# Performance work log

Measured on AMD Instinct MI355X. Metric: run time of the kernel, lower is better.

Reference implementation:

```python
import jax, jax.numpy as jnp
import numpy as np

NUM_HEADS = 16
ROPE_BASE = 10000.0
MAX_POS = 4096


def _rope_tables(head_dim):
    inv_freq = 1.0 / (ROPE_BASE ** (np.arange(0, head_dim, 2, dtype=np.float32) / head_dim))
    freqs = np.arange(MAX_POS, dtype=np.float32)[:, None] * inv_freq[None, :]
    emb = np.concatenate([freqs, freqs], axis=-1)  # [MAX_POS, head_dim]
    return jnp.asarray(np.cos(emb)), jnp.asarray(np.sin(emb))


def _rotate_half(x):
    d = x.shape[-1] // 2
    return jnp.concatenate([-x[..., d:], x[..., :d]], axis=-1)


def _apply_rope(x, pos, cos_t, sin_t):
    # x: [B,H,S,D], pos: [B,S]
    cos = cos_t[pos][:, None]  # [B,1,S,D]
    sin = sin_t[pos][:, None]
    return x * cos + _rotate_half(x) * sin


def setup_inputs() -> dict:
    key = jax.random.key(0)
    ks = jax.random.split(key, 8)
    B, N, M, C = 2, 2048, 2048, 1024
    s = 1.0 / np.sqrt(C)
    return {
        "query": jax.random.normal(ks[0], (B, N, C), jnp.float32),
        "key": jax.random.normal(ks[1], (B, M, C), jnp.float32),
        "query_pos": jnp.broadcast_to(jnp.arange(N, dtype=jnp.int32), (B, N)),
        "key_pos": jnp.broadcast_to(jnp.arange(M, dtype=jnp.int32), (B, M)),
        "Wq": jax.random.normal(ks[2], (C, C), jnp.float32) * s,
        "bq": jnp.zeros((C,), jnp.float32),
        "Wk": jax.random.normal(ks[3], (C, C), jnp.float32) * s,
        "Wv": jax.random.normal(ks[4], (C, C), jnp.float32) * s,
        "bv": jnp.zeros((C,), jnp.float32),
        "Wo": jax.random.normal(ks[5], (C, C), jnp.float32) * s,
        "bo": jnp.zeros((C,), jnp.float32),
    }


def reference(query, key, query_pos, key_pos, Wq, bq, Wk, Wv, bv, Wo, bo):
    B, N, C = query.shape
    M = key.shape[1]
    H = NUM_HEADS
    D = C // H
    scale = D ** -0.5
    cos_t, sin_t = _rope_tables(D)

    value = key  # value defaults to key
    identity = query

    q = (query @ Wq.T + bq).reshape(B, N, H, D).transpose(0, 2, 1, 3)
    k = (key @ Wk.T).reshape(B, M, H, D).transpose(0, 2, 1, 3)
    v = (value @ Wv.T + bv).reshape(B, M, H, D).transpose(0, 2, 1, 3)

    q = _apply_rope(q, query_pos, cos_t, sin_t)
    k = _apply_rope(k, key_pos, cos_t, sin_t)

    attn = jnp.einsum('bhnd,bhmd->bhnm', q, k) * scale
    attn = jax.nn.softmax(attn, axis=-1)
    x = jnp.einsum('bhnm,bhmd->bhnd', attn, v)  # [B,H,N,D]
    x = x.transpose(0, 2, 1, 3).reshape(B, N, C)
    x = x @ Wo.T + bo
    return x + identity
```

## Files before the change

### kernel.cpp

```cpp
#include <hip/hip_runtime.h>
#include <hip/hip_bf16.h>
#include <stdint.h>

#define B_ 2
#define N_ 2048
#define M_ 2048
#define C_ 1024
#define H_ 16
#define D_ 64

typedef __attribute__((ext_vector_type(8))) short s16x8;
typedef __attribute__((ext_vector_type(4))) short s16x4;
typedef __attribute__((ext_vector_type(4))) float f32x4;
typedef __attribute__((ext_vector_type(16))) float f32x16;

__device__ __attribute__((always_inline)) inline short f2b(float f){
    __hip_bfloat16 h = __float2bfloat16(f); short s; __builtin_memcpy(&s, &h, 2); return s;
}
__device__ __attribute__((always_inline)) inline float b2f(short s){
    __hip_bfloat16 h; __builtin_memcpy(&h, &s, 2); return __bfloat162float(h);
}

#define MFMA16(a,b,c) __builtin_amdgcn_mfma_f32_16x16x32_bf16(a,b,c,0,0,0)
#define MFMA32(a,b,c) __builtin_amdgcn_mfma_f32_32x32x16_bf16(a,b,c,0,0,0)

__device__ __attribute__((always_inline)) inline void gl_lds16(const void* g, void* l){
    __builtin_amdgcn_global_load_lds((__attribute__((address_space(1))) void*)g,
                                     (__attribute__((address_space(3))) void*)l, 16, 0, 0);
}
__device__ __attribute__((always_inline)) inline unsigned fbits(float f){
    unsigned u; __builtin_memcpy(&u, &f, 4); return u;
}
__device__ __attribute__((always_inline)) inline unsigned cvtpk(float lo, float hi){
    unsigned r;
    asm("v_cvt_pk_bf16_f32 %0, %1, %2" : "=v"(r) : "v"(lo), "v"(hi));
    return r;
}
__device__ __attribute__((always_inline)) inline void lane32swap(unsigned &a, unsigned &b){
    asm("v_permlane32_swap_b32 %0, %1" : "+v"(a), "+v"(b));
}

__global__ void cvt_all(const float* __restrict__ q, const float* __restrict__ k,
                        const float* __restrict__ wq, const float* __restrict__ wk,
                        const float* __restrict__ wv, const float* __restrict__ wo,
                        short* __restrict__ dst){
    long i = ((long)blockIdx.x * 256 + threadIdx.x) * 8;
    const float* src; long off;
    if      (i <  4194304L){ src = q;  off = i; }
    else if (i <  8388608L){ src = k;  off = i - 4194304L; }
    else if (i <  9437184L){ src = wq; off = i - 8388608L; }
    else if (i < 10485760L){ src = wk; off = i - 9437184L; }
    else if (i < 11534336L){ src = wv; off = i - 10485760L; }
    else                   { src = wo; off = i - 11534336L; }
    float4 a = *(const float4*)(src + off);
    float4 b = *(const float4*)(src + off + 4);
    s16x8 o;
    o[0]=f2b(a.x); o[1]=f2b(a.y); o[2]=f2b(a.z); o[3]=f2b(a.w);
    o[4]=f2b(b.x); o[5]=f2b(b.y); o[6]=f2b(b.z); o[7]=f2b(b.w);
    *(s16x8*)(dst + i) = o;
}

__global__ __launch_bounds__(256, 3) void gemm_qkv(
    const short* __restrict__ qbf, const short* __restrict__ kbf,
    const short* __restrict__ W,
    const float* __restrict__ bq, const float* __restrict__ bv,
    short* __restrict__ qproj, short* __restrict__ kproj, short* __restrict__ vT)
{
    __shared__ short As[128 * 32];
    __shared__ short Bs[128 * 32];
    const int n0 = blockIdx.x * 128, m0 = blockIdx.y * 128;
    const int sel = n0 >> 10;
    const short* A = (sel == 0) ? qbf : kbf;
    const int tid = threadIdx.x, lane = tid & 63, wave = tid >> 6;
    const int quad = lane >> 4, l16 = lane & 15;
    const int wr = (wave >> 1) * 64, wc = (wave & 1) * 64;
    const int srow = lane >> 2, scol = (lane & 3) * 8;

    f32x4 acc[4][4] = {};

    const short* Ag = A + (size_t)(m0 + wave * 32 + srow) * C_ + scol;
    const short* Bg = W + (size_t)(n0 + wave * 32 + srow) * C_ + scol;
    short* lA0 = As + (wave * 32) * 32;
    short* lA1 = As + (wave * 32 + 16) * 32;
    short* lB0 = Bs + (wave * 32) * 32;
    short* lB1 = Bs + (wave * 32 + 16) * 32;

    for (int k0 = 0; k0 < C_; k0 += 32){
        __syncthreads();
        gl_lds16(Ag + k0, lA0);
        gl_lds16(Ag + k0 + 16 * (size_t)C_, lA1);
        gl_lds16(Bg + k0, lB0);
        gl_lds16(Bg + k0 + 16 * (size_t)C_, lB1);
        __syncthreads();
        s16x8 af[4], bfr[4];
        #pragma unroll
        for (int t = 0; t < 4; t++) af[t]  = *(const s16x8*)&As[(wr + t*16 + l16) * 32 + quad * 8];
        #pragma unroll
        for (int t = 0; t < 4; t++) bfr[t] = *(const s16x8*)&Bs[(wc + t*16 + l16) * 32 + quad * 8];
        #pragma unroll
        for (int i = 0; i < 4; i++)
            #pragma unroll
            for (int j = 0; j < 4; j++)
                acc[i][j] = MFMA16(af[i], bfr[j], acc[i][j]);
    }

    if (sel <= 1){
        short* dst = sel ? kproj : qproj;
        const float* bp = sel ? nullptr : bq;
        const int coff = sel << 10;
        #pragma unroll
        for (int j = 0; j < 4; j++){
            int c = n0 + wc + j * 16 + l16 - coff;
            float bb = bp ? bp[c] : 0.0f;
            #pragma unroll
            for (int i = 0; i < 4; i++){
                int row = m0 + wr + i * 16 + quad * 4;
                #pragma unroll
                for (int r = 0; r < 4; r++)
                    dst[(size_t)(row + r) * C_ + c] = f2b(acc[i][j][r] + bb);
            }
        }
    } else {
        #pragma unroll
        for (int j = 0; j < 4; j++){
            int col = n0 - 2048 + wc + j * 16 + l16;
            int h = col >> 6, d = col & 63;
            float bb = bv[col];
            #pragma unroll
            for (int i = 0; i < 4; i++){
                int row = m0 + wr + i * 16 + quad * 4;
                int b = row >> 11, m = row & 2047;
                unsigned u0 = (unsigned)(unsigned short)f2b(acc[i][j][0] + bb) |
                              ((unsigned)(unsigned short)f2b(acc[i][j][1] + bb) << 16);
                unsigned u1 = (unsigned)(unsigned short)f2b(acc[i][j][2] + bb) |
                              ((unsigned)(unsigned short)f2b(acc[i][j][3] + bb) << 16);
                uint2 u; u.x = u0; u.y = u1;
                *(uint2*)&vT[(((size_t)(b * H_ + h)) * D_ + d) * M_ + m] = u;
            }
        }
    }
}

__global__ __launch_bounds__(256, 4) void gemm_out(
    const short* __restrict__ A, const short* __restrict__ W,
    const float* __restrict__ bias, const float* __restrict__ resid,
    float* __restrict__ outf)
{
    __shared__ short As[128 * 32];
    __shared__ short Bs[64 * 32];
    const int n0 = blockIdx.x * 64, m0 = blockIdx.y * 128;
    const int tid = threadIdx.x, lane = tid & 63, wave = tid >> 6;
    const int quad = lane >> 4, l16 = lane & 15;
    const int srow = lane >> 2, scol = (lane & 3) * 8;

    f32x4 acc[2][4] = {};
    const short* Ag = A + (size_t)(m0 + wave * 32 + srow) * C_ + scol;
    const short* Bg = W + (size_t)(n0 + wave * 16 + srow) * C_ + scol;
    short* lA0 = As + (wave * 32) * 32;
    short* lA1 = As + (wave * 32 + 16) * 32;
    short* lB  = Bs + (wave * 16) * 32;

    for (int k0 = 0; k0 < C_; k0 += 32){
        __syncthreads();
        gl_lds16(Ag + k0, lA0);
        gl_lds16(Ag + k0 + 16 * (size_t)C_, lA1);
        gl_lds16(Bg + k0, lB);
        __syncthreads();
        s16x8 af[2], bfr[4];
        #pragma unroll
        for (int t = 0; t < 2; t++) af[t]  = *(const s16x8*)&As[(wave*32 + t*16 + l16) * 32 + quad * 8];
        #pragma unroll
        for (int t = 0; t < 4; t++) bfr[t] = *(const s16x8*)&Bs[(t*16 + l16) * 32 + quad * 8];
        #pragma unroll
        for (int i = 0; i < 2; i++)
            #pragma unroll
            for (int j = 0; j < 4; j++)
                acc[i][j] = MFMA16(af[i], bfr[j], acc[i][j]);
    }

    #pragma unroll
    for (int j = 0; j < 4; j++){
        int c = n0 + j * 16 + l16;
        float bb = bias[c];
        #pragma unroll
        for (int i = 0; i < 2; i++){
            int row = m0 + wave * 32 + i * 16 + quad * 4;
            #pragma unroll
            for (int r = 0; r < 4; r++){
                size_t idx = (size_t)(row + r) * C_ + c;
                outf[idx] = acc[i][j][r] + bb + resid[idx];
            }
        }
    }
}

__global__ void rope_k(short* __restrict__ k, const int* __restrict__ kpos){
    int t = blockIdx.x * blockDim.x + threadIdx.x;
    int i = t & 31;
    int h = (t >> 5) & (H_ - 1);
    int row = t >> 9;
    int pos = kpos[row];
    short* base = k + (size_t)row * C_ + h * D_;
    float x1 = b2f(base[i]), x2 = b2f(base[i + 32]);
    float invf = exp2f((float)i * (-13.287712379549449f / 32.0f));
    float f = (float)pos * invf;
    float c = __cosf(f), s = __sinf(f);
    base[i]      = f2b(x1 * c - x2 * s);
    base[i + 32] = f2b(x2 * c + x1 * s);
}

__global__ __launch_bounds__(256, 2) void flash_attn(
    const short* __restrict__ q, const short* __restrict__ k,
    const short* __restrict__ vt, short* __restrict__ o,
    const int* __restrict__ qpos)
{
    __shared__ short smem[17920];
    const int b = blockIdx.y >> 4, h = blockIdx.y & 15;
    const int n0 = blockIdx.x * 128;
    const int tid = threadIdx.x, lane = tid & 63, wave = tid >> 6;
    const int hi = lane >> 5, l32 = lane & 31;
    const int wq = wave & 1, kq = wave >> 1;

    s16x8 qf[2][4];
    const float fac = 0.18033688011112042f;
    #pragma unroll
    for (int qt = 0; qt < 2; qt++){
        int qrow = n0 + wq * 64 + qt * 32 + l32;
        const short* qg = &q[((size_t)(b * N_ + qrow)) * C_ + h * D_];
        float pos = (float)qpos[b * N_ + qrow];
        s16x8 raw[4];
        #pragma unroll
        for (int c = 0; c < 4; c++) raw[c] = *(const s16x8*)&qg[c * 16 + hi * 8];
        #pragma unroll
        for (int c = 0; c < 2; c++){
            s16x8 olo, ohi8;
            #pragma unroll
            for (int j = 0; j < 8; j++){
                int irot = c * 16 + hi * 8 + j;
                float invf = exp2f((float)irot * (-13.287712379549449f / 32.0f));
                float ang = pos * invf;
                float cs = __cosf(ang), sn = __sinf(ang);
                float x1 = b2f(raw[c][j]), x2 = b2f(raw[c + 2][j]);
                olo[j]  = f2b((x1 * cs - x2 * sn) * fac);
                ohi8[j] = f2b((x2 * cs + x1 * sn) * fac);
            }
            qf[qt][c] = olo; qf[qt][c + 2] = ohi8;
        }
    }

    const short* kg = k  + (size_t)(b * M_) * C_ + h * D_;
    const short* vg = vt + ((size_t)(b * H_ + h)) * D_ * M_;
    const int srow0 = tid >> 3, sseg = (tid & 7) * 8;

    union V8 { s16x8 v; uint2 u[2]; };
    V8 kreg[2], vreg[2];

    #pragma unroll
    for (int ii = 0; ii < 2; ii++){
        int row = srow0 + 32 * ii;
        kreg[ii].v = *(const s16x8*)&kg[(size_t)row * C_ + sseg];
        vreg[ii].v = *(const s16x8*)&vg[(size_t)row * M_ + sseg];
    }
    #pragma unroll
    for (int ii = 0; ii < 2; ii++){
        int row = srow0 + 32 * ii;
        short* kd = &smem[row * 68 + sseg];
        *(uint2*)kd = kreg[ii].u[0]; *(uint2*)(kd + 4) = kreg[ii].u[1];
        short* vd = &smem[8704 + row * 68 + sseg];
        *(uint2*)vd = vreg[ii].u[0]; *(uint2*)(vd + 4) = vreg[ii].u[1];
    }

    f32x16 zero16 = {};
    f32x16 oacc[2][2] = {zero16, zero16, zero16, zero16};
    float lacc[2] = {0.f, 0.f};

    for (int st = 0; st < 32; st++){
        const int p = st & 1;
        __syncthreads();
        if (st < 31){
            #pragma unroll
            for (int ii = 0; ii < 2; ii++){
                int row = srow0 + 32 * ii;
                kreg[ii].v = *(const s16x8*)&kg[((size_t)((st + 1) * 64 + row)) * C_ + sseg];
                vreg[ii].v = *(const s16x8*)&vg[(size_t)row * M_ + (st + 1) * 64 + sseg];
            }
        }
        const short* Kp = &smem[p * 4352];
        const short* Vp = &smem[8704 + p * 4352];

        s16x4 kf[4][2];
        #pragma unroll
        for (int c = 0; c < 4; c++){
            const short* a = &Kp[(kq * 32 + l32) * 68 + c * 16 + hi * 8];
            kf[c][0] = *(const s16x4*)a; kf[c][1] = *(const s16x4*)(a + 4);
        }
        s16x8 vf[2][2];
        #pragma unroll
        for (int dt = 0; dt < 2; dt++)
            #pragma unroll
            for (int c = 0; c < 2; c++){
                const short* a = &Vp[(dt * 32 + l32) * 68 + kq * 32 + c * 16 + hi * 8];
                vf[dt][c] = __builtin_shufflevector(*(const s16x4*)a, *(const s16x4*)(a + 4),
                                                    0,1,2,3,4,5,6,7);
            }

        s16x8 pf[2][2];
        #pragma unroll
        for (int qt = 0; qt < 2; qt++){
            f32x16 sv = {};
            #pragma unroll
            for (int c = 0; c < 4; c++){
                s16x8 ka = __builtin_shufflevector(kf[c][0], kf[c][1], 0,1,2,3,4,5,6,7);
                sv = MFMA32(ka, qf[qt][c], sv);
            }
            float pe[16];
            #pragma unroll
            for (int e = 0; e < 16; e++) pe[e] = __builtin_amdgcn_exp2f(sv[e]);
            float ls = 0.f;
            #pragma unroll
            for (int e = 0; e < 16; e += 4) ls += (pe[e] + pe[e+1]) + (pe[e+2] + pe[e+3]);
            lacc[qt] += ls;
            #pragma unroll
            for (int c = 0; c < 2; c++){
                unsigned a1 = cvtpk(pe[8*c + 0], pe[8*c + 1]);
                unsigned a2 = cvtpk(pe[8*c + 2], pe[8*c + 3]);
                unsigned b1 = cvtpk(pe[8*c + 4], pe[8*c + 5]);
                unsigned b2 = cvtpk(pe[8*c + 6], pe[8*c + 7]);
                lane32swap(a1, b1);
                lane32swap(a2, b2);
                union { unsigned u[4]; s16x8 v; } pk;
                pk.u[0] = a1; pk.u[1] = a2; pk.u[2] = b1; pk.u[3] = b2;
                pf[qt][c] = pk.v;
            }
        }

        #pragma unroll
        for (int qt = 0; qt < 2; qt++)
            #pragma unroll
            for (int dt = 0; dt < 2; dt++)
                #pragma unroll
                for (int c = 0; c < 2; c++)
                    oacc[qt][dt] = MFMA32(pf[qt][c], vf[dt][c], oacc[qt][dt]);

        if (st < 31){
            int pn = p ^ 1;
            #pragma unroll
            for (int ii = 0; ii < 2; ii++){
                int row = srow0 + 32 * ii;
                short* kd = &smem[pn * 4352 + row * 68 + sseg];
                *(uint2*)kd = kreg[ii].u[0]; *(uint2*)(kd + 4) = kreg[ii].u[1];
                short* vd = &smem[8704 + pn * 4352 + row * 68 + sseg];
                *(uint2*)vd = vreg[ii].u[0]; *(uint2*)(vd + 4) = vreg[ii].u[1];
            }
        }
    }

    __syncthreads();

    float* LO   = (float*)smem;
    float* Lsum = (float*)&smem[17408];
    float* Linv = Lsum + 128;

    float l0[2];
    #pragma unroll
    for (int qt = 0; qt < 2; qt++)
        l0[qt] = lacc[qt] + __shfl_xor(lacc[qt], 32);

    if (kq == 1){
        #pragma unroll
        for (int qt = 0; qt < 2; qt++)
            Lsum[wq * 64 + qt * 32 + l32] = l0[qt];
        #pragma unroll
        for (int qt = 0; qt < 2; qt++)
            #pragma unroll
            for (int dt = 0; dt < 2; dt++)
                #pragma unroll
                for (int e = 0; e < 16; e++){
                    int qrow = wq * 64 + qt * 32 + (e & 3) + 8 * (e >> 2) + 4 * hi;
                    LO[qrow * 65 + dt * 32 + l32] = oacc[qt][dt][e];
                }
    }
    __syncthreads();
    if (kq == 0){
        #pragma unroll
        for (int qt = 0; qt < 2; qt++){
            float lt = l0[qt] + Lsum[wq * 64 + qt * 32 + l32];
            Linv[wq * 64 + qt * 32 + l32] = 1.0f / lt;
        }
        asm volatile("s_waitcnt lgkmcnt(0)" ::: "memory");
        #pragma unroll
        for (int qt = 0; qt < 2; qt++)
            #pragma unroll
            for (int dt = 0; dt < 2; dt++)
                #pragma unroll
                for (int e = 0; e < 16; e++){
                    int qrow = wq * 64 + qt * 32 + (e & 3) + 8 * (e >> 2) + 4 * hi;
                    float val = (oacc[qt][dt][e] + LO[qrow * 65 + dt * 32 + l32]) * Linv[qrow];
                    o[((size_t)(b * N_ + n0 + qrow)) * C_ + h * D_ + dt * 32 + l32] = f2b(val);
                }
    }
}

extern "C" void kernel_launch(void* const* d_in, const int* in_sizes, int n_in,
                              void* d_out, int out_size, void* d_ws, size_t ws_size,
                              hipStream_t stream) {
    const float* query = (const float*)d_in[0];
    const float* key   = (const float*)d_in[1];
    const int*   qpos  = (const int*)d_in[2];
    const int*   kpos  = (const int*)d_in[3];
    const float* Wq    = (const float*)d_in[4];
    const float* bq    = (const float*)d_in[5];
    const float* Wk    = (const float*)d_in[6];
    const float* Wv    = (const float*)d_in[7];
    const float* bv    = (const float*)d_in[8];
    const float* Wo    = (const float*)d_in[9];
    const float* bo    = (const float*)d_in[10];
    float* out = (float*)d_out;

    const size_t E4M = (size_t)4 * 1024 * 1024;
    const size_t E1M = (size_t)1024 * 1024;
    short* ws    = (short*)d_ws;
    short* qbf   = ws;
    short* kbf   = qbf   + E4M;
    short* wqkvb = kbf   + E4M;
    short* wob   = wqkvb + 3 * E1M;
    short* qproj = wob   + E1M;
    short* kproj = qproj + E4M;
    short* vT    = kproj + E4M;
    short* attn  = qbf;

    cvt_all<<<6144, 256, 0, stream>>>(query, key, Wq, Wk, Wv, Wo, ws);

    gemm_qkv<<<dim3(24, 32), 256, 0, stream>>>(qbf, kbf, wqkvb, bq, bv,
                                               qproj, kproj, vT);

    rope_k<<<(B_ * M_ * H_ * 32) / 256, 256, 0, stream>>>(kproj, kpos);

    flash_attn<<<dim3(16, 32), 256, 0, stream>>>(qproj, kproj, vT, attn, qpos);

    gemm_out<<<dim3(16, 32), 256, 0, stream>>>(attn, wob, bo, query, out);
}
```

Baseline: 210.8 us.

## Halve flash-attention query tile to 64 rows and double grid occupancy

Each flash_attn block now processes 64 query rows instead of 128, with each wave handling a single 32-row query tile. The grid doubles to 1024 blocks and launch bounds request 4 blocks per CU, lowering register pressure and raising occupancy. The cost is that K/V tiles are streamed from global memory twice as often per query row, so each loaded K/V tile is reused over half as many MFMAs.

```diff
diff --git a/kernel.cpp b/kernel.cpp
--- a/kernel.cpp
+++ b/kernel.cpp
@@ -209,23 +209,22 @@
     base[i + 32] = f2b(x2 * c + x1 * s);
 }
 
-__global__ __launch_bounds__(256, 2) void flash_attn(
+__global__ __launch_bounds__(256, 4) void flash_attn(
     const short* __restrict__ q, const short* __restrict__ k,
     const short* __restrict__ vt, short* __restrict__ o,
     const int* __restrict__ qpos)
 {
     __shared__ short smem[17920];
     const int b = blockIdx.y >> 4, h = blockIdx.y & 15;
-    const int n0 = blockIdx.x * 128;
+    const int n0 = blockIdx.x * 64;
     const int tid = threadIdx.x, lane = tid & 63, wave = tid >> 6;
     const int hi = lane >> 5, l32 = lane & 31;
     const int wq = wave & 1, kq = wave >> 1;
 
-    s16x8 qf[2][4];
+    s16x8 qf[4];
     const float fac = 0.18033688011112042f;
-    #pragma unroll
-    for (int qt = 0; qt < 2; qt++){
-        int qrow = n0 + wq * 64 + qt * 32 + l32;
+    {
+        int qrow = n0 + wq * 32 + l32;
         const short* qg = &q[((size_t)(b * N_ + qrow)) * C_ + h * D_];
         float pos = (float)qpos[b * N_ + qrow];
         s16x8 raw[4];
@@ -244,7 +243,7 @@
                 olo[j]  = f2b((x1 * cs - x2 * sn) * fac);
                 ohi8[j] = f2b((x2 * cs + x1 * sn) * fac);
             }
-            qf[qt][c] = olo; qf[qt][c + 2] = ohi8;
+            qf[c] = olo; qf[c + 2] = ohi8;
         }
     }
 
@@ -271,8 +270,8 @@
     }
 
     f32x16 zero16 = {};
-    f32x16 oacc[2][2] = {zero16, zero16, zero16, zero16};
-    float lacc[2] = {0.f, 0.f};
+    f32x16 oacc[2] = {zero16, zero16};
+    float lacc = 0.f;
 
     for (int st = 0; st < 32; st++){
         const int p = st & 1;
@@ -304,43 +303,38 @@
                                                     0,1,2,3,4,5,6,7);
             }
 
-        s16x8 pf[2][2];
-        #pragma unroll
-        for (int qt = 0; qt < 2; qt++){
-            f32x16 sv = {};
-            #pragma unroll
-            for (int c = 0; c < 4; c++){
-                s16x8 ka = __builtin_shufflevector(kf[c][0], kf[c][1], 0,1,2,3,4,5,6,7);
-                sv = MFMA32(ka, qf[qt][c], sv);
-            }
-            float pe[16];
-            #pragma unroll
-            for (int e = 0; e < 16; e++) pe[e] = __builtin_amdgcn_exp2f(sv[e]);
-            float ls = 0.f;
-            #pragma unroll
-            for (int e = 0; e < 16; e += 4) ls += (pe[e] + pe[e+1]) + (pe[e+2] + pe[e+3]);
-            lacc[qt] += ls;
-            #pragma unroll
-            for (int c = 0; c < 2; c++){
-                unsigned a1 = cvtpk(pe[8*c + 0], pe[8*c + 1]);
-                unsigned a2 = cvtpk(pe[8*c + 2], pe[8*c + 3]);
-                unsigned b1 = cvtpk(pe[8*c + 4], pe[8*c + 5]);
-                unsigned b2 = cvtpk(pe[8*c + 6], pe[8*c + 7]);
-                lane32swap(a1, b1);
-                lane32swap(a2, b2);
-                union { unsigned u[4]; s16x8 v; } pk;
-                pk.u[0] = a1; pk.u[1] = a2; pk.u[2] = b1; pk.u[3] = b2;
-                pf[qt][c] = pk.v;
-            }
-        }
-
-        #pragma unroll
-        for (int qt = 0; qt < 2; qt++)
-            #pragma unroll
-            for (int dt = 0; dt < 2; dt++)
-                #pragma unroll
-                for (int c = 0; c < 2; c++)
-                    oacc[qt][dt] = MFMA32(pf[qt][c], vf[dt][c], oacc[qt][dt]);
+        f32x16 sv = {};
+        #pragma unroll
+        for (int c = 0; c < 4; c++){
+            s16x8 ka = __builtin_shufflevector(kf[c][0], kf[c][1], 0,1,2,3,4,5,6,7);
+            sv = MFMA32(ka, qf[c], sv);
+        }
+        float pe[16];
+        #pragma unroll
+        for (int e = 0; e < 16; e++) pe[e] = __builtin_amdgcn_exp2f(sv[e]);
+        float ls = 0.f;
+        #pragma unroll
+        for (int e = 0; e < 16; e += 4) ls += (pe[e] + pe[e+1]) + (pe[e+2] + pe[e+3]);
+        lacc += ls;
+        s16x8 pf[2];
+        #pragma unroll
+        for (int c = 0; c < 2; c++){
+            unsigned a1 = cvtpk(pe[8*c + 0], pe[8*c + 1]);
+            unsigned a2 = cvtpk(pe[8*c + 2], pe[8*c + 3]);
+            unsigned b1 = cvtpk(pe[8*c + 4], pe[8*c + 5]);
+            unsigned b2 = cvtpk(pe[8*c + 6], pe[8*c + 7]);
+            lane32swap(a1, b1);
+            lane32swap(a2, b2);
+            union { unsigned u[4]; s16x8 v; } pk;
+            pk.u[0] = a1; pk.u[1] = a2; pk.u[2] = b1; pk.u[3] = b2;
+            pf[c] = pk.v;
+        }
+
+        #pragma unroll
+        for (int dt = 0; dt < 2; dt++)
+            #pragma unroll
+            for (int c = 0; c < 2; c++)
+                oacc[dt] = MFMA32(pf[c], vf[dt][c], oacc[dt]);
 
         if (st < 31){
             int pn = p ^ 1;
@@ -359,45 +353,33 @@
 
     float* LO   = (float*)smem;
     float* Lsum = (float*)&smem[17408];
-    float* Linv = Lsum + 128;
-
-    float l0[2];
-    #pragma unroll
-    for (int qt = 0; qt < 2; qt++)
-        l0[qt] = lacc[qt] + __shfl_xor(lacc[qt], 32);
+    float* Linv = Lsum + 64;
+
+    float l0 = lacc + __shfl_xor(lacc, 32);
 
     if (kq == 1){
-        #pragma unroll
-        for (int qt = 0; qt < 2; qt++)
-            Lsum[wq * 64 + qt * 32 + l32] = l0[qt];
-        #pragma unroll
-        for (int qt = 0; qt < 2; qt++)
-            #pragma unroll
-            for (int dt = 0; dt < 2; dt++)
-                #pragma unroll
-                for (int e = 0; e < 16; e++){
-                    int qrow = wq * 64 + qt * 32 + (e & 3) + 8 * (e >> 2) + 4 * hi;
-                    LO[qrow * 65 + dt * 32 + l32] = oacc[qt][dt][e];
-                }
+        Lsum[wq * 32 + l32] = l0;
+        #pragma unroll
+        for (int dt = 0; dt < 2; dt++)
+            #pragma unroll
+            for (int e = 0; e < 16; e++){
+                int qrow = wq * 32 + (e & 3) + 8 * (e >> 2) + 4 * hi;
+                LO[qrow * 65 + dt * 32 + l32] = oacc[dt][e];
+            }
     }
     __syncthreads();
     if (kq == 0){
-        #pragma unroll
-        for (int qt = 0; qt < 2; qt++){
-            float lt = l0[qt] + Lsum[wq * 64 + qt * 32 + l32];
-            Linv[wq * 64 + qt * 32 + l32] = 1.0f / lt;
-        }
+        float lt = l0 + Lsum[wq * 32 + l32];
+        Linv[wq * 32 + l32] = 1.0f / lt;
         asm volatile("s_waitcnt lgkmcnt(0)" ::: "memory");
         #pragma unroll
-        for (int qt = 0; qt < 2; qt++)
-            #pragma unroll
-            for (int dt = 0; dt < 2; dt++)
-                #pragma unroll
-                for (int e = 0; e < 16; e++){
-                    int qrow = wq * 64 + qt * 32 + (e & 3) + 8 * (e >> 2) + 4 * hi;
-                    float val = (oacc[qt][dt][e] + LO[qrow * 65 + dt * 32 + l32]) * Linv[qrow];
-                    o[((size_t)(b * N_ + n0 + qrow)) * C_ + h * D_ + dt * 32 + l32] = f2b(val);
-                }
+        for (int dt = 0; dt < 2; dt++)
+            #pragma unroll
+            for (int e = 0; e < 16; e++){
+                int qrow = wq * 32 + (e & 3) + 8 * (e >> 2) + 4 * hi;
+                float val = (oacc[dt][e] + LO[qrow * 65 + dt * 32 + l32]) * Linv[qrow];
+                o[((size_t)(b * N_ + n0 + qrow)) * C_ + h * D_ + dt * 32 + l32] = f2b(val);
+            }
     }
 }
 
@@ -436,7 +418,7 @@
 
     rope_k<<<(B_ * M_ * H_ * 32) / 256, 256, 0, stream>>>(kproj, kpos);
 
-    flash_attn<<<dim3(16, 32), 256, 0, stream>>>(qproj, kproj, vT, attn, qpos);
+    flash_attn<<<dim3(32, 32), 256, 0, stream>>>(qproj, kproj, vT, attn, qpos);
 
     gemm_out<<<dim3(16, 32), 256, 0, stream>>>(attn, wob, bo, query, out);
 }
```

After: 220.9 us. 1.05x slower.
